# Optimization experiments

Hardware: AMD Instinct MI355X
Metric: run time of the kernel (lower is better)

Reference implementation:

```python
import jax, jax.numpy as jnp
import numpy as np

DIM_MODEL = 512
DIM_HEAD = 64


def setup_inputs() -> dict:
    key = jax.random.key(0)
    ks = jax.random.split(key, 7)
    B, S = 4, 4096
    x = jax.random.normal(ks[0], (B, S, DIM_MODEL), dtype=jnp.float32)
    mask = jnp.ones((B, 1, S), dtype=jnp.int32)
    # torch Linear init: U(-1/sqrt(fan_in), 1/sqrt(fan_in)); stored as (in, out) for x @ W
    bound = 1.0 / np.sqrt(DIM_MODEL)
    Wq = jax.random.uniform(ks[1], (DIM_MODEL, DIM_HEAD), minval=-bound, maxval=bound, dtype=jnp.float32)
    bq = jax.random.uniform(ks[2], (DIM_HEAD,), minval=-bound, maxval=bound, dtype=jnp.float32)
    Wk = jax.random.uniform(ks[3], (DIM_MODEL, DIM_HEAD), minval=-bound, maxval=bound, dtype=jnp.float32)
    bk = jax.random.uniform(ks[4], (DIM_HEAD,), minval=-bound, maxval=bound, dtype=jnp.float32)
    Wv = jax.random.uniform(ks[5], (DIM_MODEL, DIM_HEAD), minval=-bound, maxval=bound, dtype=jnp.float32)
    bv = jax.random.uniform(ks[6], (DIM_HEAD,), minval=-bound, maxval=bound, dtype=jnp.float32)
    return {"x": x, "mask": mask, "Wq": Wq, "bq": bq, "Wk": Wk, "bk": bk, "Wv": Wv, "bv": bv}


def reference(x, mask, Wq, bq, Wk, bk, Wv, bv):
    # single-head QKV projection
    q = x @ Wq + bq  # (B, S, Dh)
    k = x @ Wk + bk
    v = x @ Wv + bv
    dot_scale = jnp.sqrt(jnp.float32(DIM_HEAD))
    # explicit O(S^2) score matrix, softmax over keys
    scores = jnp.einsum("bqd,bkd->bqk", q, k) / dot_scale  # (B, S, S)
    attn = jax.nn.softmax(scores, axis=-1)
    # faithful to source: mask applied AFTER softmax with -inf fill
    attn = jnp.where(mask == 0, jnp.float32(-jnp.inf), attn)
    return jnp.einsum("bqk,bkd->bqd", attn, v)  # (B, S, Dh)
```

## Files before the change

kernel.cpp:

```cpp
#include <hip/hip_runtime.h>
#include <hip/hip_bf16.h>

typedef _Float16 half8v __attribute__((ext_vector_type(8)));
typedef _Float16 half4v __attribute__((ext_vector_type(4)));
typedef _Float16 half2v __attribute__((ext_vector_type(2)));
typedef __fp16   fp16x2 __attribute__((ext_vector_type(2)));
typedef __attribute__((ext_vector_type(4))) float floatx4;

#define LOG2E_OVER_8 0.18033688011112042f

#if __has_builtin(__builtin_amdgcn_exp2f)
#define EXP2(x) __builtin_amdgcn_exp2f(x)
#else
#define EXP2(x) exp2f(x)
#endif


__device__ __forceinline__ void gload_lds16(const void* g, void* l) {
    __builtin_amdgcn_global_load_lds(
        (const __attribute__((address_space(1))) void*)(unsigned long long)g,
        (__attribute__((address_space(3))) void*)(unsigned)(unsigned long long)l,
        16, 0, 0);
}

__global__ __launch_bounds__(256) void wtrans_k(const float* __restrict__ Wq,
                                                const float* __restrict__ Wk,
                                                const float* __restrict__ Wv,
                                                _Float16* __restrict__ Wt) {
    int idx = blockIdx.x * 256 + threadIdx.x;
    int p = idx >> 15, rem = idx & 32767;
    int k = rem >> 6;
    int n = rem & 63;
    const float* W = (p == 0) ? Wq : ((p == 1) ? Wk : Wv);
    int ctg = p * 4 + (n >> 4), m = n & 15;
    int kc = k >> 5, quad = (k >> 3) & 3, j = k & 7;
    Wt[(((ctg << 4) + kc) * 64 + (quad << 4) + m) * 8 + j] = (_Float16)W[k * 64 + n];
}

#define XS_STRIDE 536
__global__ __launch_bounds__(256) void proj_k(const float* __restrict__ x,
                                              const _Float16* __restrict__ Wt,
                                              const float* __restrict__ bq,
                                              const float* __restrict__ bk,
                                              const float* __restrict__ bv,
                                              _Float16* __restrict__ Qh,
                                              _Float16* __restrict__ Kh,
                                              _Float16* __restrict__ Vh) {
    __shared__ _Float16 xs[2][16 * XS_STRIDE];

    int tid = threadIdx.x, l = tid & 63, wv = tid >> 6;
    int m = l & 15, quad = l >> 4;
    int row0 = blockIdx.x * 32;

#pragma unroll
    for (int s = 0; s < 2; s++)
#pragma unroll
        for (int i = 0; i < 8; i++) {
            int idx = tid + i * 256;
            int row = idx >> 7, c4 = idx & 127;
            float4 v = *(const float4*)(x + (row0 + s * 16 + row) * 512 + c4 * 4);
            union { half2v h[2]; uint2 u; } cv;
            cv.h[0][0] = (_Float16)v.x; cv.h[0][1] = (_Float16)v.y;
            cv.h[1][0] = (_Float16)v.z; cv.h[1][1] = (_Float16)v.w;
            *(uint2*)(xs[s] + row * XS_STRIDE + c4 * 4) = cv.u;
        }
    __syncthreads();

    const _Float16* arow0 = xs[0] + m * XS_STRIDE + quad * 8;
    const _Float16* arow1 = xs[1] + m * XS_STRIDE + quad * 8;

    floatx4 acc[2][3];
#pragma unroll
    for (int s = 0; s < 2; s++)
#pragma unroll
        for (int i = 0; i < 3; i++) acc[s][i] = (floatx4)(0.f);

#pragma unroll 4
    for (int kc = 0; kc < 16; kc++) {
        half8v a0 = *(const half8v*)(arow0 + kc * 32);
        half8v a1 = *(const half8v*)(arow1 + kc * 32);
#pragma unroll
        for (int ct = 0; ct < 3; ct++) {
            int ctg = wv * 3 + ct;
            half8v b = *(const half8v*)(Wt + (((ctg << 4) + kc) * 64 + l) * 8);
            acc[0][ct] = __builtin_amdgcn_mfma_f32_16x16x32_f16(a0, b, acc[0][ct], 0, 0, 0);
            acc[1][ct] = __builtin_amdgcn_mfma_f32_16x16x32_f16(a1, b, acc[1][ct], 0, 0, 0);
        }
    }

#pragma unroll
    for (int s = 0; s < 2; s++) {
        int rowb = row0 + s * 16;
#pragma unroll
        for (int ct = 0; ct < 3; ct++) {
            int ctg = wv * 3 + ct;
            int col = ctg * 16 + m;
            float bias = (ctg < 4) ? bq[col] : ((ctg < 8) ? bk[col - 64] : bv[col - 128]);
            if (ctg < 8) {
                _Float16* dst = (ctg < 4) ? Qh : Kh;
                float scl = (ctg < 4) ? LOG2E_OVER_8 : 1.0f;
                int dd = (ctg & 3) * 16 + m;
                int c = dd >> 5, quadQ = (dd >> 3) & 3, j = dd & 7;
#pragma unroll
                for (int r = 0; r < 4; r++) {
                    int row = rowb + quad * 4 + r;
                    int chunk = ((row >> 4) << 1) + c;
                    dst[(chunk * 64 + quadQ * 16 + (row & 15)) * 8 + j] =
                        (_Float16)((acc[s][ct][r] + bias) * scl);
                }
            } else {
                int dt = ctg - 8;
                int t64 = rowb >> 6, ktp = (rowb >> 5) & 1, half = (rowb >> 4) & 1;
                int chunk = t64 * 8 + dt * 2 + ktp;
                union { _Float16 h[4]; unsigned long long u; } pk;
#pragma unroll
                for (int r = 0; r < 4; r++) pk.h[r] = (_Float16)(acc[s][ct][r] + bias);
                *(unsigned long long*)(Vh + (chunk * 64 + quad * 16 + m) * 8 + half * 4) = pk.u;
            }
        }
    }
}

template <int NT>
__global__ __launch_bounds__(256, 4) void attn_k(const _Float16* __restrict__ Qh,
                                                 const _Float16* __restrict__ Kh,
                                                 const _Float16* __restrict__ Vh,
                                                 const int* __restrict__ mask,
                                                 _Float16* __restrict__ Np,
                                                 float* __restrict__ Dp,
                                                 int gshift) {
    __shared__ __align__(16) uint4 stage_lds[2][1024];

    int tid = threadIdx.x, l = tid & 63, wv = tid >> 6;
    int m = l & 15, quad = l >> 4;
    int bid = blockIdx.x;
    int grp = bid & ((1 << gshift) - 1), qblk = bid >> gshift;
    int os = grp >> 2, b = grp & 3;
    int q0 = qblk * 128 + wv * 32;

    const int* maskb = mask + b * 4096 + os * (NT * 64);
    int az = 0;
#pragma unroll
    for (int i = 0; i < NT; i++) az |= (maskb[l + i * 64] == 0);
    const bool hasz = __any(az);

    int qt_g = (b * 4096 + q0) >> 4;
    half8v qf[2][2];
#pragma unroll
    for (int qt = 0; qt < 2; qt++)
#pragma unroll
        for (int c = 0; c < 2; c++)
            qf[qt][c] = *(const half8v*)(Qh + (((qt_g + qt) * 2 + c) * 64 + l) * 8);

    half8v ones8;
#pragma unroll
    for (int i = 0; i < 8; i++) ones8[i] = (_Float16)1.0f;

    int tb0 = (b * 64 + os * NT) * 512;
    const uint4* kh4 = (const uint4*)Kh + tb0;
    const uint4* vh4 = (const uint4*)Vh + tb0;

    floatx4 oacc[2][4];
#pragma unroll
    for (int qt = 0; qt < 2; qt++)
#pragma unroll
        for (int dt = 0; dt < 4; dt++) oacc[qt][dt] = (floatx4)(0.f);
    floatx4 oden[2] = {(floatx4)(0.f), (floatx4)(0.f)};

#pragma unroll
    for (int i = 0; i < 2; i++) {
        int idx = wv * 128 + i * 64 + l;
        gload_lds16(kh4 + idx, &stage_lds[0][0] + idx);
        gload_lds16(vh4 + idx, &stage_lds[0][512] + idx);
    }
    __syncthreads();

    for (int t = 0; t < NT; t++) {
        int cur = t & 1;
        if (t + 1 < NT) {
            const uint4* ksrc = kh4 + (t + 1) * 512;
            const uint4* vsrc = vh4 + (t + 1) * 512;
            uint4* kb = &stage_lds[cur ^ 1][0];
            uint4* vb = &stage_lds[cur ^ 1][512];
#pragma unroll
            for (int i = 0; i < 2; i++) {
                int idx = wv * 128 + i * 64 + l;
                gload_lds16(ksrc + idx, kb + idx);
                gload_lds16(vsrc + idx, vb + idx);
            }
        }
        const uint4* kt4 = &stage_lds[cur][0];
        const uint4* vt4 = &stage_lds[cur][512];
#pragma unroll
        for (int sp = 0; sp < 2; sp++) {
            union { uint4 u; half8v h; } kk[4];
#pragma unroll
            for (int i = 0; i < 4; i++)
                kk[i].u = kt4[(sp * 4 + i) * 64 + l];
            uint4 vv[4];
#pragma unroll
            for (int dt = 0; dt < 4; dt++)
                vv[dt] = vt4[(dt * 2 + sp) * 64 + l];
            half8v pb8[2];
#pragma unroll
            for (int qt = 0; qt < 2; qt++) {
                union { fp16x2 h2[4]; half8v h8; } pu;
#pragma unroll
                for (int se = 0; se < 2; se++) {
                    floatx4 sf = (floatx4)(0.f);
                    __builtin_amdgcn_s_setprio(1);
                    sf = __builtin_amdgcn_mfma_f32_16x16x32_f16(kk[se * 2 + 0].h, qf[qt][0], sf, 0, 0, 0);
                    sf = __builtin_amdgcn_mfma_f32_16x16x32_f16(kk[se * 2 + 1].h, qf[qt][1], sf, 0, 0, 0);
                    __builtin_amdgcn_s_setprio(0);
                    float p0 = EXP2(sf[0]), p1 = EXP2(sf[1]);
                    float p2 = EXP2(sf[2]), p3 = EXP2(sf[3]);
                    if (hasz) {
                        int kg = t * 64 + (sp * 2 + se) * 16 + quad * 4;
                        if (maskb[kg + 0] == 0) p0 = -__builtin_inff();
                        if (maskb[kg + 1] == 0) p1 = -__builtin_inff();
                        if (maskb[kg + 2] == 0) p2 = -__builtin_inff();
                        if (maskb[kg + 3] == 0) p3 = -__builtin_inff();
                    }
                    pu.h2[se * 2 + 0] = __builtin_amdgcn_cvt_pkrtz(p0, p1);
                    pu.h2[se * 2 + 1] = __builtin_amdgcn_cvt_pkrtz(p2, p3);
                }
                pb8[qt] = pu.h8;
            }
            __builtin_amdgcn_s_setprio(1);
            oden[0] = __builtin_amdgcn_mfma_f32_16x16x32_f16(ones8, pb8[0], oden[0], 0, 0, 0);
            oden[1] = __builtin_amdgcn_mfma_f32_16x16x32_f16(ones8, pb8[1], oden[1], 0, 0, 0);
#pragma unroll
            for (int dt = 0; dt < 4; dt++) {
                union { uint4 u; half8v h; } vc; vc.u = vv[dt];
                oacc[0][dt] = __builtin_amdgcn_mfma_f32_16x16x32_f16(vc.h, pb8[0], oacc[0][dt], 0, 0, 0);
                oacc[1][dt] = __builtin_amdgcn_mfma_f32_16x16x32_f16(vc.h, pb8[1], oacc[1][dt], 0, 0, 0);
            }
            __builtin_amdgcn_s_setprio(0);
        }
        __syncthreads();
    }

    float* Tw = (float*)&stage_lds[0][0] + wv * (16 * 68);
    int rowb = os * 16384 + b * 4096 + q0;
#pragma unroll
    for (int qt = 0; qt < 2; qt++) {
        if (l < 16) Dp[rowb + qt * 16 + l] = oden[qt][0];
#pragma unroll
        for (int dt = 0; dt < 4; dt++)
#pragma unroll
            for (int r = 0; r < 4; r++)
                Tw[m * 68 + dt * 16 + quad * 4 + r] = oacc[qt][dt][r];
        asm volatile("s_waitcnt lgkmcnt(0)" ::: "memory");
        __builtin_amdgcn_sched_barrier(0);
#pragma unroll
        for (int g = 0; g < 4; g++) {
            int idx = g * 64 + l;
            int row = idx >> 4, c4 = (idx & 15) * 4;
            float4 v = *(const float4*)(Tw + row * 68 + c4);
            union { half4v h; unsigned long long u; } pk;
            pk.h[0] = (_Float16)v.x; pk.h[1] = (_Float16)v.y;
            pk.h[2] = (_Float16)v.z; pk.h[3] = (_Float16)v.w;
            *(unsigned long long*)(Np + (size_t)(rowb + qt * 16 + row) * 64 + c4) = pk.u;
        }
        asm volatile("s_waitcnt lgkmcnt(0)" ::: "memory");
        __builtin_amdgcn_sched_barrier(0);
    }
}

__global__ __launch_bounds__(256) void combine_k(const _Float16* __restrict__ Np,
                                                 const float* __restrict__ Dp,
                                                 float* __restrict__ out,
                                                 int spl) {
    int g4 = blockIdx.x * 256 + threadIdx.x;
    int row = g4 >> 4;
    float4 nu = make_float4(0.f, 0.f, 0.f, 0.f);
    float d = 0.f;
    for (int sp = 0; sp < spl; sp++) {
        union { unsigned long long u; half4v h; } v;
        v.u = *(const unsigned long long*)(Np + ((size_t)sp << 20) + (size_t)g4 * 4);
        nu.x += (float)v.h[0]; nu.y += (float)v.h[1];
        nu.z += (float)v.h[2]; nu.w += (float)v.h[3];
        d += Dp[sp * 16384 + row];
    }
    float inv = 1.0f / d;
    ((float4*)out)[g4] = make_float4(nu.x * inv, nu.y * inv, nu.z * inv, nu.w * inv);
}

extern "C" void kernel_launch(void* const* d_in, const int* in_sizes, int n_in,
                              void* d_out, int out_size, void* d_ws, size_t ws_size,
                              hipStream_t stream) {
    const float* x  = (const float*)d_in[0];
    const int* mask = (const int*)d_in[1];
    const float* Wq = (const float*)d_in[2];
    const float* bq = (const float*)d_in[3];
    const float* Wk = (const float*)d_in[4];
    const float* bk = (const float*)d_in[5];
    const float* Wv = (const float*)d_in[6];
    const float* bv = (const float*)d_in[7];
    float* out = (float*)d_out;

    char* ws = (char*)d_ws;
    _Float16* Wt = (_Float16*)(ws);
    _Float16* Qh = (_Float16*)(ws + 0x40000);
    _Float16* Kh = (_Float16*)(ws + 0x240000);
    _Float16* Vh = (_Float16*)(ws + 0x440000);
    float*    Dp = (float*)(ws + 0x640000);
    _Float16* Np = (_Float16*)(ws + 0x740000);

    wtrans_k<<<384, 256, 0, stream>>>(Wq, Wk, Wv, Wt);
    proj_k<<<512, 256, 0, stream>>>(x, Wt, bq, bk, bv, Qh, Kh, Vh);
    attn_k<8><<<32 * 32, 256, 0, stream>>>(Qh, Kh, Vh, mask, Np, Dp, 5);
    combine_k<<<1024, 256, 0, stream>>>(Np, Dp, out, 8);
}
```

Baseline: 122.1 us.

## Halve per-wave query rows and double key-split length in attention kernel

Each wave now handles one 16-row query tile instead of two, so each block covers 64 query rows. The key dimension is split 4 ways instead of 8, with 16 key tiles per split, and the grid stays at 1024 blocks. This cuts register pressure and the partial numerator/denominator traffic into the combine kernel. In exchange, each staged K/V tile is reused across fewer query rows, so every block loads more K/V from global memory.

```diff
diff --git a/kernel.cpp b/kernel.cpp
--- a/kernel.cpp
+++ b/kernel.cpp
@@ -136,7 +136,7 @@
     int bid = blockIdx.x;
     int grp = bid & ((1 << gshift) - 1), qblk = bid >> gshift;
     int os = grp >> 2, b = grp & 3;
-    int q0 = qblk * 128 + wv * 32;
+    int q0 = qblk * 64 + wv * 16;
 
     const int* maskb = mask + b * 4096 + os * (NT * 64);
     int az = 0;
@@ -145,12 +145,10 @@
     const bool hasz = __any(az);
 
     int qt_g = (b * 4096 + q0) >> 4;
-    half8v qf[2][2];
-#pragma unroll
-    for (int qt = 0; qt < 2; qt++)
-#pragma unroll
-        for (int c = 0; c < 2; c++)
-            qf[qt][c] = *(const half8v*)(Qh + (((qt_g + qt) * 2 + c) * 64 + l) * 8);
+    half8v qf[2];
+#pragma unroll
+    for (int c = 0; c < 2; c++)
+        qf[c] = *(const half8v*)(Qh + ((qt_g * 2 + c) * 64 + l) * 8);
 
     half8v ones8;
 #pragma unroll
@@ -160,12 +158,10 @@
     const uint4* kh4 = (const uint4*)Kh + tb0;
     const uint4* vh4 = (const uint4*)Vh + tb0;
 
-    floatx4 oacc[2][4];
-#pragma unroll
-    for (int qt = 0; qt < 2; qt++)
-#pragma unroll
-        for (int dt = 0; dt < 4; dt++) oacc[qt][dt] = (floatx4)(0.f);
-    floatx4 oden[2] = {(floatx4)(0.f), (floatx4)(0.f)};
+    floatx4 oacc[4];
+#pragma unroll
+    for (int dt = 0; dt < 4; dt++) oacc[dt] = (floatx4)(0.f);
+    floatx4 oden = (floatx4)(0.f);
 
 #pragma unroll
     for (int i = 0; i < 2; i++) {
@@ -201,16 +197,15 @@
 #pragma unroll
             for (int dt = 0; dt < 4; dt++)
                 vv[dt] = vt4[(dt * 2 + sp) * 64 + l];
-            half8v pb8[2];
-#pragma unroll
-            for (int qt = 0; qt < 2; qt++) {
+            half8v pb8;
+            {
                 union { fp16x2 h2[4]; half8v h8; } pu;
 #pragma unroll
                 for (int se = 0; se < 2; se++) {
                     floatx4 sf = (floatx4)(0.f);
                     __builtin_amdgcn_s_setprio(1);
-                    sf = __builtin_amdgcn_mfma_f32_16x16x32_f16(kk[se * 2 + 0].h, qf[qt][0], sf, 0, 0, 0);
-                    sf = __builtin_amdgcn_mfma_f32_16x16x32_f16(kk[se * 2 + 1].h, qf[qt][1], sf, 0, 0, 0);
+                    sf = __builtin_amdgcn_mfma_f32_16x16x32_f16(kk[se * 2 + 0].h, qf[0], sf, 0, 0, 0);
+                    sf = __builtin_amdgcn_mfma_f32_16x16x32_f16(kk[se * 2 + 1].h, qf[1], sf, 0, 0, 0);
                     __builtin_amdgcn_s_setprio(0);
                     float p0 = EXP2(sf[0]), p1 = EXP2(sf[1]);
                     float p2 = EXP2(sf[2]), p3 = EXP2(sf[3]);
@@ -224,16 +219,14 @@
                     pu.h2[se * 2 + 0] = __builtin_amdgcn_cvt_pkrtz(p0, p1);
                     pu.h2[se * 2 + 1] = __builtin_amdgcn_cvt_pkrtz(p2, p3);
                 }
-                pb8[qt] = pu.h8;
+                pb8 = pu.h8;
             }
             __builtin_amdgcn_s_setprio(1);
-            oden[0] = __builtin_amdgcn_mfma_f32_16x16x32_f16(ones8, pb8[0], oden[0], 0, 0, 0);
-            oden[1] = __builtin_amdgcn_mfma_f32_16x16x32_f16(ones8, pb8[1], oden[1], 0, 0, 0);
+            oden = __builtin_amdgcn_mfma_f32_16x16x32_f16(ones8, pb8, oden, 0, 0, 0);
 #pragma unroll
             for (int dt = 0; dt < 4; dt++) {
                 union { uint4 u; half8v h; } vc; vc.u = vv[dt];
-                oacc[0][dt] = __builtin_amdgcn_mfma_f32_16x16x32_f16(vc.h, pb8[0], oacc[0][dt], 0, 0, 0);
-                oacc[1][dt] = __builtin_amdgcn_mfma_f32_16x16x32_f16(vc.h, pb8[1], oacc[1][dt], 0, 0, 0);
+                oacc[dt] = __builtin_amdgcn_mfma_f32_16x16x32_f16(vc.h, pb8, oacc[dt], 0, 0, 0);
             }
             __builtin_amdgcn_s_setprio(0);
         }
@@ -242,28 +235,23 @@
 
     float* Tw = (float*)&stage_lds[0][0] + wv * (16 * 68);
     int rowb = os * 16384 + b * 4096 + q0;
-#pragma unroll
-    for (int qt = 0; qt < 2; qt++) {
-        if (l < 16) Dp[rowb + qt * 16 + l] = oden[qt][0];
-#pragma unroll
-        for (int dt = 0; dt < 4; dt++)
-#pragma unroll
-            for (int r = 0; r < 4; r++)
-                Tw[m * 68 + dt * 16 + quad * 4 + r] = oacc[qt][dt][r];
-        asm volatile("s_waitcnt lgkmcnt(0)" ::: "memory");
-        __builtin_amdgcn_sched_barrier(0);
-#pragma unroll
-        for (int g = 0; g < 4; g++) {
-            int idx = g * 64 + l;
-            int row = idx >> 4, c4 = (idx & 15) * 4;
-            float4 v = *(const float4*)(Tw + row * 68 + c4);
-            union { half4v h; unsigned long long u; } pk;
-            pk.h[0] = (_Float16)v.x; pk.h[1] = (_Float16)v.y;
-            pk.h[2] = (_Float16)v.z; pk.h[3] = (_Float16)v.w;
-            *(unsigned long long*)(Np + (size_t)(rowb + qt * 16 + row) * 64 + c4) = pk.u;
-        }
-        asm volatile("s_waitcnt lgkmcnt(0)" ::: "memory");
-        __builtin_amdgcn_sched_barrier(0);
+    if (l < 16) Dp[rowb + l] = oden[0];
+#pragma unroll
+    for (int dt = 0; dt < 4; dt++)
+#pragma unroll
+        for (int r = 0; r < 4; r++)
+            Tw[m * 68 + dt * 16 + quad * 4 + r] = oacc[dt][r];
+    asm volatile("s_waitcnt lgkmcnt(0)" ::: "memory");
+    __builtin_amdgcn_sched_barrier(0);
+#pragma unroll
+    for (int g = 0; g < 4; g++) {
+        int idx = g * 64 + l;
+        int row = idx >> 4, c4 = (idx & 15) * 4;
+        float4 v = *(const float4*)(Tw + row * 68 + c4);
+        union { half4v h; unsigned long long u; } pk;
+        pk.h[0] = (_Float16)v.x; pk.h[1] = (_Float16)v.y;
+        pk.h[2] = (_Float16)v.z; pk.h[3] = (_Float16)v.w;
+        *(unsigned long long*)(Np + (size_t)(rowb + row) * 64 + c4) = pk.u;
     }
 }
 
@@ -309,6 +297,6 @@
 
     wtrans_k<<<384, 256, 0, stream>>>(Wq, Wk, Wv, Wt);
     proj_k<<<512, 256, 0, stream>>>(x, Wt, bq, bk, bv, Qh, Kh, Vh);
-    attn_k<8><<<32 * 32, 256, 0, stream>>>(Qh, Kh, Vh, mask, Np, Dp, 5);
-    combine_k<<<1024, 256, 0, stream>>>(Np, Dp, out, 8);
-}
+    attn_k<16><<<64 * 16, 256, 0, stream>>>(Qh, Kh, Vh, mask, Np, Dp, 4);
+    combine_k<<<1024, 256, 0, stream>>>(Np, Dp, out, 4);
+}
```

Measured after the change: 123.0 us. No clear change (+0.8%).
